# Kernel tuning notes

Measured on AMD Instinct MI355X. Metric: run time of the kernel, lower is better.

## Reference

```python
import jax, jax.numpy as jnp
import numpy as np

N = 20000
E = 320000
HID = 64
HEADS = 4
OUT = 64
NEG_SLOPE = 0.2


def gat_conv(x, src, dst, W, a_src, a_dst, b, heads, out_ch, n_nodes):
    # Linear transform then split heads: [N, heads, out_ch]
    h = (x @ W).reshape(n_nodes, heads, out_ch)
    # Per-node attention logits (PyG GATConv): alpha_i = <h_i, a>
    alpha_s = (h * a_src).sum(-1)  # [N, heads]
    alpha_d = (h * a_dst).sum(-1)  # [N, heads]
    # Edge-wise raw scores e_{j->i} = LeakyReLU(alpha_s[j] + alpha_d[i])
    e = jax.nn.leaky_relu(alpha_s[src] + alpha_d[dst], NEG_SLOPE)  # [E, heads]
    # Segment softmax over incoming edges of each destination node
    m = jax.ops.segment_max(e, dst, num_segments=n_nodes)  # [N, heads]
    ex = jnp.exp(e - m[dst])
    s = jax.ops.segment_sum(ex, dst, num_segments=n_nodes)  # [N, heads]
    alpha = ex / (s[dst] + 1e-16)  # [E, heads]
    # Weighted scatter-add aggregation
    msg = h[src] * alpha[..., None]  # [E, heads, out_ch]
    out = jax.ops.segment_sum(msg, dst, num_segments=n_nodes)
    return out.reshape(n_nodes, heads * out_ch) + b


def setup_inputs() -> dict:
    key = jax.random.key(0)
    ks = jax.random.split(key, 16)
    sc = lambda fi, fo: 1.0 / np.sqrt(fi)
    x = jax.random.normal(ks[0], (N, HID), dtype=jnp.float32)
    edge_index = jax.random.randint(ks[1], (2, E), 0, N, dtype=jnp.int32)
    d = dict(x=x, edge_index=edge_index)
    # layer 1: HID -> HID, HEADS heads (concat)
    d['W1'] = jax.random.normal(ks[2], (HID, HEADS * HID), jnp.float32) * sc(HID, HEADS * HID)
    d['a1s'] = jax.random.normal(ks[3], (HEADS, HID), jnp.float32) * 0.1
    d['a1d'] = jax.random.normal(ks[4], (HEADS, HID), jnp.float32) * 0.1
    d['b1'] = jnp.zeros((HEADS * HID,), jnp.float32)
    # layer 2: HEADS*HID -> HID, HEADS heads (concat)
    d['W2'] = jax.random.normal(ks[5], (HEADS * HID, HEADS * HID), jnp.float32) * sc(HEADS * HID, HEADS * HID)
    d['a2s'] = jax.random.normal(ks[6], (HEADS, HID), jnp.float32) * 0.1
    d['a2d'] = jax.random.normal(ks[7], (HEADS, HID), jnp.float32) * 0.1
    d['b2'] = jnp.zeros((HEADS * HID,), jnp.float32)
    # layer 3: HEADS*HID -> OUT, 1 head
    d['W3'] = jax.random.normal(ks[8], (HEADS * HID, OUT), jnp.float32) * sc(HEADS * HID, OUT)
    d['a3s'] = jax.random.normal(ks[9], (1, OUT), jnp.float32) * 0.1
    d['a3d'] = jax.random.normal(ks[10], (1, OUT), jnp.float32) * 0.1
    d['b3'] = jnp.zeros((OUT,), jnp.float32)
    return d


def reference(x, edge_index, W1, a1s, a1d, b1, W2, a2s, a2d, b2, W3, a3s, a3d, b3):
    src, dst = edge_index[0], edge_index[1]
    h = jax.nn.relu(gat_conv(x, src, dst, W1, a1s, a1d, b1, HEADS, HID, N))
    h = jax.nn.relu(gat_conv(h, src, dst, W2, a2s, a2d, b2, HEADS, HID, N))
    out = gat_conv(h, src, dst, W3, a3s, a3d, b3, 1, OUT, N)
    return out
```

## Files before the change

kernel.cpp:

```cpp
#include <hip/hip_runtime.h>
#include <hip/hip_bf16.h>
#include <hip/hip_fp16.h>
#include <cstdint>

#define HID 64
#define NHEADS 4
#define NEG_SLOPE 0.2f

typedef __attribute__((ext_vector_type(8))) short short8;
typedef __attribute__((ext_vector_type(4))) short short4v;
typedef __attribute__((ext_vector_type(16))) float f32x16;
typedef unsigned short us;

__device__ __forceinline__ us f2bf(float f) {
    unsigned int u = __float_as_uint(f);
    unsigned int r = (u + 0x7FFFu + ((u >> 16) & 1u)) >> 16;
    return (us)r;
}
__device__ __forceinline__ float bf2f(us h) {
    return __uint_as_float(((unsigned int)h) << 16);
}
__device__ __forceinline__ float leaky(float e) {
    return (e > 0.f) ? e : NEG_SLOPE * e;
}

__global__ void histo_kernel(const int* __restrict__ dst, int* __restrict__ counts, int E) {
    int i = blockIdx.x * blockDim.x + threadIdx.x;
    if (i < E) atomicAdd(&counts[dst[i]], 1);
}

__global__ __launch_bounds__(256) void scanA_kernel(const int* __restrict__ counts,
                                                    int* __restrict__ bsum, int n) {
    const int i = blockIdx.x * 256 + threadIdx.x;
    int v = (i < n) ? counts[i] : 0;
#pragma unroll
    for (int o = 32; o; o >>= 1) v += __shfl_xor(v, o);
    __shared__ int ws[4];
    if ((threadIdx.x & 63) == 0) ws[threadIdx.x >> 6] = v;
    __syncthreads();
    if (threadIdx.x == 0) bsum[blockIdx.x] = ws[0] + ws[1] + ws[2] + ws[3];
}

__global__ __launch_bounds__(256) void scanC_kernel(const int* __restrict__ counts,
                                                    const int* __restrict__ bsum,
                                                    int* __restrict__ offs,
                                                    int* __restrict__ wp, int n, int nb) {
    __shared__ int sh[256];
    __shared__ int shb[256];
    const int t = threadIdx.x;
    shb[t] = (t < nb) ? bsum[t] : 0;
    __syncthreads();
    for (int o = 1; o < 256; o <<= 1) {
        int u = (t >= o) ? shb[t - o] : 0;
        __syncthreads();
        shb[t] += u;
        __syncthreads();
    }
    const int base = (blockIdx.x == 0) ? 0 : shb[blockIdx.x - 1];
    const int i = blockIdx.x * 256 + t;
    const int v = (i < n) ? counts[i] : 0;
    sh[t] = v;
    __syncthreads();
    for (int o = 1; o < 256; o <<= 1) {
        int u = (t >= o) ? sh[t - o] : 0;
        __syncthreads();
        sh[t] += u;
        __syncthreads();
    }
    if (i < n) {
        const int off = base + sh[t] - v;
        offs[i] = off;
        wp[i] = off;
        if (i == n - 1) offs[n] = base + sh[t];
    }
}

__global__ void scatter_kernel(const int* __restrict__ src, const int* __restrict__ dst,
                               int* __restrict__ wp, int* __restrict__ csr, int E) {
    int i = blockIdx.x * blockDim.x + threadIdx.x;
    if (i < E) {
        int d = dst[i];
        int p = atomicAdd(&wp[d], 1);
        csr[p] = src[i];
    }
}

__device__ __forceinline__ void wsplit_one(const float* __restrict__ W, us* __restrict__ WTh,
                                           us* __restrict__ WTl, int K, int OUTC, int i) {
    const int c = i / K;
    const int k = i - c * K;
    const float v = W[(size_t)k * OUTC + c];
    const us h = f2bf(v);
    WTh[i] = h;
    WTl[i] = f2bf(v - bf2f(h));
}

__device__ __forceinline__ void vaprep_one(const float* __restrict__ W,
                                           const float* __restrict__ as,
                                           const float* __restrict__ ad,
                                           us* __restrict__ vh, us* __restrict__ vl,
                                           int K, int OUTC, int H, int i) {
    const int j = i / K;
    const int k = i - j * K;
    const int hh = (j < 4) ? j : j - 4;
    const float* a = (j < 4) ? as : ad;
    float acc = 0.f;
    if (hh < H) {
        for (int c = 0; c < 64; ++c)
            acc += W[(size_t)k * OUTC + hh * 64 + c] * a[hh * 64 + c];
    }
    const us h = f2bf(acc);
    vh[i] = h;
    vl[i] = f2bf(acc - bf2f(h));
}

__global__ __launch_bounds__(256) void prep_kernel(
    const float* x, int nx,
    const float* W1, const float* W2, const float* W3,
    const float* a1s, const float* a1d, const float* a2s, const float* a2d,
    const float* a3s, const float* a3d,
    us* xh, us* xl,
    us* wt1h, us* wt1l, us* wt2h, us* wt2l, us* wt3h, us* wt3l,
    us* va1h, us* va1l, us* va2h, us* va2l, us* va3h, us* va3l) {
    int idx = blockIdx.x * 256 + threadIdx.x;
    if (idx < nx) {
        const float v = x[idx];
        const us h = f2bf(v);
        xh[idx] = h;
        xl[idx] = f2bf(v - bf2f(h));
        return;
    }
    idx -= nx;
    if (idx < 16384) { wsplit_one(W1, wt1h, wt1l, 64, 256, idx); return; }
    idx -= 16384;
    if (idx < 65536) { wsplit_one(W2, wt2h, wt2l, 256, 256, idx); return; }
    idx -= 65536;
    if (idx < 16384) { wsplit_one(W3, wt3h, wt3l, 256, 64, idx); return; }
    idx -= 16384;
    if (idx < 512) { vaprep_one(W1, a1s, a1d, va1h, va1l, 64, 256, 4, idx); return; }
    idx -= 512;
    if (idx < 2048) { vaprep_one(W2, a2s, a2d, va2h, va2l, 256, 256, 4, idx); return; }
    idx -= 2048;
    if (idx < 2048) { vaprep_one(W3, a3s, a3d, va3h, va3l, 256, 64, 1, idx); return; }
}

template <int K, int OUTC, int BN, int HA>
__global__ __launch_bounds__(256) void gemm_mfma_kernel(const us* __restrict__ AH,
                                                        const us* __restrict__ AL,
                                                        const us* __restrict__ WTh,
                                                        const us* __restrict__ WTl,
                                                        const us* __restrict__ vah,
                                                        const us* __restrict__ val,
                                                        _Float16* __restrict__ H16,
                                                        float* __restrict__ alpha_s,
                                                        float* __restrict__ alpha_d, int nrows) {
    constexpr int CGS = BN / 64;
    constexpr int NB = BN / 64;
    constexpr int TPC = 4 / NB;
    __shared__ short Ah[2 * 64 * 32];
    __shared__ short Al[2 * 64 * 32];
    __shared__ short Bh[2 * BN * 32];
    __shared__ short Bl[2 * BN * 32];
    __shared__ short Vh[2 * 8 * 32];
    __shared__ short Vl[2 * 8 * 32];

    const int tid = threadIdx.x;
    const int lane = tid & 63;
    const int wid = tid >> 6;
    const int wr = wid >> 1;
    const int wc = wid & 1;
    const int r31 = lane & 31;
    const int khw = lane >> 5;
    const int row0 = blockIdx.x * 64;
    const int c0 = blockIdx.y * BN;
    const bool alpha_blk = (blockIdx.y == 0);
    const bool alpha_wave = alpha_blk && (wc == 0);

    const int ar = tid >> 2;
    const int akb = tid & 3;
    const bool aok = (row0 + ar) < nrows;
    const int bcol = tid / TPC;
    const int bkb = (tid % TPC) * NB;

    f32x16 acc[CGS];
#pragma unroll
    for (int cg = 0; cg < CGS; ++cg)
#pragma unroll
        for (int r = 0; r < 16; ++r) acc[cg][r] = 0.f;
    f32x16 accv;
#pragma unroll
    for (int r = 0; r < 16; ++r) accv[r] = 0.f;

    for (int k0 = 0; k0 < K; k0 += 64) {
        __syncthreads();
#pragma unroll
        for (int sub = 0; sub < 2; ++sub) {
            {
                short8 h = {}, l = {};
                if (aok) {
                    const size_t so = (size_t)(row0 + ar) * K + k0 + sub * 32 + akb * 8;
                    h = *reinterpret_cast<const short8*>(&AH[so]);
                    l = *reinterpret_cast<const short8*>(&AL[so]);
                }
                const int off = sub * 2048 + ar * 32 + ((akb ^ (ar & 3)) << 3);
                *reinterpret_cast<short8*>(&Ah[off]) = h;
                *reinterpret_cast<short8*>(&Al[off]) = l;
            }
            {
                const us* srcH = &WTh[(size_t)(c0 + bcol) * K + k0 + sub * 32];
                const us* srcL = &WTl[(size_t)(c0 + bcol) * K + k0 + sub * 32];
#pragma unroll
                for (int b = 0; b < NB; ++b) {
                    short8 h = *reinterpret_cast<const short8*>(&srcH[(bkb + b) * 8]);
                    short8 l = *reinterpret_cast<const short8*>(&srcL[(bkb + b) * 8]);
                    const int off = sub * BN * 32 + bcol * 32 + (((bkb + b) ^ (bcol & 3)) << 3);
                    *reinterpret_cast<short8*>(&Bh[off]) = h;
                    *reinterpret_cast<short8*>(&Bl[off]) = l;
                }
            }
            if (alpha_blk && tid < 32) {
                const int col = tid >> 2, kb2 = tid & 3;
                const int off = sub * 256 + col * 32 + kb2 * 8;
                *reinterpret_cast<short8*>(&Vh[off]) =
                    *reinterpret_cast<const short8*>(&vah[col * K + k0 + sub * 32 + kb2 * 8]);
                *reinterpret_cast<short8*>(&Vl[off]) =
                    *reinterpret_cast<const short8*>(&val[col * K + k0 + sub * 32 + kb2 * 8]);
            }
        }
        __syncthreads();
#pragma unroll
        for (int sub = 0; sub < 2; ++sub) {
#pragma unroll
            for (int ks = 0; ks < 32; ks += 16) {
                const int kb = (ks >> 3) + khw;
                const int aoff = sub * 2048 + (wr * 32 + r31) * 32 + ((kb ^ (r31 & 3)) << 3);
                short8 ah = *reinterpret_cast<const short8*>(&Ah[aoff]);
                short8 al = *reinterpret_cast<const short8*>(&Al[aoff]);
#pragma unroll
                for (int cg = 0; cg < CGS; ++cg) {
                    const int coll = wc * (BN / 2) + cg * 32 + r31;
                    const int boff = sub * BN * 32 + coll * 32 + ((kb ^ (r31 & 3)) << 3);
                    short8 bh = *reinterpret_cast<const short8*>(&Bh[boff]);
                    short8 bl = *reinterpret_cast<const short8*>(&Bl[boff]);
                    acc[cg] = __builtin_amdgcn_mfma_f32_32x32x16_bf16(ah, bh, acc[cg], 0, 0, 0);
                    acc[cg] = __builtin_amdgcn_mfma_f32_32x32x16_bf16(ah, bl, acc[cg], 0, 0, 0);
                    acc[cg] = __builtin_amdgcn_mfma_f32_32x32x16_bf16(al, bh, acc[cg], 0, 0, 0);
                }
                if (alpha_wave) {
                    short8 vh = {}, vl = {};
                    if (r31 < 8) {
                        const int voff = sub * 256 + r31 * 32 + (kb << 3);
                        vh = *reinterpret_cast<const short8*>(&Vh[voff]);
                        vl = *reinterpret_cast<const short8*>(&Vl[voff]);
                    }
                    accv = __builtin_amdgcn_mfma_f32_32x32x16_bf16(ah, vh, accv, 0, 0, 0);
                    accv = __builtin_amdgcn_mfma_f32_32x32x16_bf16(ah, vl, accv, 0, 0, 0);
                    accv = __builtin_amdgcn_mfma_f32_32x32x16_bf16(al, vh, accv, 0, 0, 0);
                }
            }
        }
    }

#pragma unroll
    for (int cg = 0; cg < CGS; ++cg) {
#pragma unroll
        for (int reg = 0; reg < 16; ++reg) {
            const int row = row0 + wr * 32 + (reg & 3) + 8 * (reg >> 2) + 4 * khw;
            if (row < nrows) {
                const int col = c0 + wc * (BN / 2) + cg * 32 + r31;
                H16[(size_t)row * OUTC + col] = (_Float16)acc[cg][reg];
            }
        }
    }
    if (alpha_wave && r31 < 8) {
        const int hsel = r31 & 3;
        if (hsel < HA) {
            float* dstp = (r31 < 4) ? alpha_s : alpha_d;
#pragma unroll
            for (int reg = 0; reg < 16; ++reg) {
                const int row = row0 + wr * 32 + (reg & 3) + 8 * (reg >> 2) + 4 * khw;
                if (row < nrows) dstp[(size_t)row * HA + hsel] = accv[reg];
            }
        }
    }
}

__global__ __launch_bounds__(64) void maxagg4_kernel(const _Float16* __restrict__ h,
                                                     const float* __restrict__ alpha_s,
                                                     const float* __restrict__ alpha_d,
                                                     const int* __restrict__ offs,
                                                     const int* __restrict__ csr,
                                                     float* __restrict__ w,
                                                     const float* __restrict__ bias,
                                                     us* __restrict__ outH,
                                                     us* __restrict__ outL, int n_nodes) {
    __shared__ float wsh[64 * 4];
    const int gw = blockIdx.x;
    const int lane = threadIdx.x;
    if (gw >= n_nodes) return;
    const int start = offs[gw];
    const int end = offs[gw + 1];
    const int deg = end - start;
    const float4 ad = *reinterpret_cast<const float4*>(&alpha_d[(size_t)gw * 4]);
    const int head = lane >> 4;
    const int cb = lane << 2;
    float4 r;
    float4 acc = make_float4(0.f, 0.f, 0.f, 0.f);

    if (deg <= 64) {
        const int i = start + lane;
        const bool has = i < end;
        int s_reg = 0;
        float4 e = make_float4(0.f, 0.f, 0.f, 0.f);
        float4 m = make_float4(-INFINITY, -INFINITY, -INFINITY, -INFINITY);
        if (has) {
            s_reg = csr[i];
            const float4 a = *reinterpret_cast<const float4*>(&alpha_s[(size_t)s_reg * 4]);
            e.x = leaky(a.x + ad.x);
            e.y = leaky(a.y + ad.y);
            e.z = leaky(a.z + ad.z);
            e.w = leaky(a.w + ad.w);
            m = e;
        }
#pragma unroll
        for (int o = 32; o; o >>= 1) {
            m.x = fmaxf(m.x, __shfl_xor(m.x, o));
            m.y = fmaxf(m.y, __shfl_xor(m.y, o));
            m.z = fmaxf(m.z, __shfl_xor(m.z, o));
            m.w = fmaxf(m.w, __shfl_xor(m.w, o));
        }
        float4 ex = make_float4(0.f, 0.f, 0.f, 0.f);
        if (has) {
            ex.x = __expf(e.x - m.x);
            ex.y = __expf(e.y - m.y);
            ex.z = __expf(e.z - m.z);
            ex.w = __expf(e.w - m.w);
        }
        float4 sum = ex;
#pragma unroll
        for (int o = 32; o; o >>= 1) {
            sum.x += __shfl_xor(sum.x, o);
            sum.y += __shfl_xor(sum.y, o);
            sum.z += __shfl_xor(sum.z, o);
            sum.w += __shfl_xor(sum.w, o);
        }
        r.x = 1.f / (sum.x + 1e-16f);
        r.y = 1.f / (sum.y + 1e-16f);
        r.z = 1.f / (sum.z + 1e-16f);
        r.w = 1.f / (sum.w + 1e-16f);
        *reinterpret_cast<float4*>(&wsh[lane * 4]) = ex;
        const int degr = (deg + 7) & ~7;
        for (int j = 0; j < degr; j += 8) {
#pragma unroll
            for (int u = 0; u < 8; ++u) {
                const int s = __shfl(s_reg, j + u);
                const float wv = wsh[(j + u) * 4 + head];
                const uint2 uv = *reinterpret_cast<const uint2*>(&h[(size_t)s * 256 + cb]);
                const float2 f0 = __half22float2(__builtin_bit_cast(__half2, uv.x));
                const float2 f1 = __half22float2(__builtin_bit_cast(__half2, uv.y));
                acc.x = fmaf(wv, f0.x, acc.x);
                acc.y = fmaf(wv, f0.y, acc.y);
                acc.z = fmaf(wv, f1.x, acc.z);
                acc.w = fmaf(wv, f1.y, acc.w);
            }
        }
    } else {
        float4 m = make_float4(-INFINITY, -INFINITY, -INFINITY, -INFINITY);
        float4 sum = make_float4(0.f, 0.f, 0.f, 0.f);
        for (int i = start + lane; i < end; i += 64) {
            const int s = csr[i];
            const float4 a = *reinterpret_cast<const float4*>(&alpha_s[(size_t)s * 4]);
            float4 e;
            e.x = leaky(a.x + ad.x);
            e.y = leaky(a.y + ad.y);
            e.z = leaky(a.z + ad.z);
            e.w = leaky(a.w + ad.w);
            *reinterpret_cast<float4*>(&w[(size_t)i * 4]) = e;
            m.x = fmaxf(m.x, e.x);
            m.y = fmaxf(m.y, e.y);
            m.z = fmaxf(m.z, e.z);
            m.w = fmaxf(m.w, e.w);
        }
#pragma unroll
        for (int o = 32; o; o >>= 1) {
            m.x = fmaxf(m.x, __shfl_xor(m.x, o));
            m.y = fmaxf(m.y, __shfl_xor(m.y, o));
            m.z = fmaxf(m.z, __shfl_xor(m.z, o));
            m.w = fmaxf(m.w, __shfl_xor(m.w, o));
        }
        for (int i = start + lane; i < end; i += 64) {
            float4 e = *reinterpret_cast<float4*>(&w[(size_t)i * 4]);
            e.x = __expf(e.x - m.x);
            e.y = __expf(e.y - m.y);
            e.z = __expf(e.z - m.z);
            e.w = __expf(e.w - m.w);
            *reinterpret_cast<float4*>(&w[(size_t)i * 4]) = e;
            sum.x += e.x;
            sum.y += e.y;
            sum.z += e.z;
            sum.w += e.w;
        }
#pragma unroll
        for (int o = 32; o; o >>= 1) {
            sum.x += __shfl_xor(sum.x, o);
            sum.y += __shfl_xor(sum.y, o);
            sum.z += __shfl_xor(sum.z, o);
            sum.w += __shfl_xor(sum.w, o);
        }
        r.x = 1.f / (sum.x + 1e-16f);
        r.y = 1.f / (sum.y + 1e-16f);
        r.z = 1.f / (sum.z + 1e-16f);
        r.w = 1.f / (sum.w + 1e-16f);
        for (int i = start; i < end; ++i) {
            const int s = csr[i];
            const float4 w0 = *reinterpret_cast<const float4*>(&w[(size_t)i * 4]);
            const float wv = head == 0 ? w0.x : head == 1 ? w0.y : head == 2 ? w0.z : w0.w;
            const uint2 uv = *reinterpret_cast<const uint2*>(&h[(size_t)s * 256 + cb]);
            const float2 f0 = __half22float2(__builtin_bit_cast(__half2, uv.x));
            const float2 f1 = __half22float2(__builtin_bit_cast(__half2, uv.y));
            acc.x = fmaf(wv, f0.x, acc.x);
            acc.y = fmaf(wv, f0.y, acc.y);
            acc.z = fmaf(wv, f1.x, acc.z);
            acc.w = fmaf(wv, f1.y, acc.w);
        }
    }

    const float rv = head == 0 ? r.x : head == 1 ? r.y : head == 2 ? r.z : r.w;
    const float4 b4 = *reinterpret_cast<const float4*>(&bias[cb]);
    float o0 = fmaxf(acc.x * rv + b4.x, 0.f);
    float o1 = fmaxf(acc.y * rv + b4.y, 0.f);
    float o2 = fmaxf(acc.z * rv + b4.z, 0.f);
    float o3 = fmaxf(acc.w * rv + b4.w, 0.f);
    short4v oh, ol;
    us t;
    t = f2bf(o0); oh[0] = (short)t; ol[0] = (short)f2bf(o0 - bf2f(t));
    t = f2bf(o1); oh[1] = (short)t; ol[1] = (short)f2bf(o1 - bf2f(t));
    t = f2bf(o2); oh[2] = (short)t; ol[2] = (short)f2bf(o2 - bf2f(t));
    t = f2bf(o3); oh[3] = (short)t; ol[3] = (short)f2bf(o3 - bf2f(t));
    *reinterpret_cast<short4v*>(&outH[(size_t)gw * 256 + cb]) = oh;
    *reinterpret_cast<short4v*>(&outL[(size_t)gw * 256 + cb]) = ol;
}

__global__ __launch_bounds__(64) void maxagg1_kernel(const _Float16* __restrict__ h,
                                                     const float* __restrict__ alpha_s,
                                                     const float* __restrict__ alpha_d,
                                                     const int* __restrict__ offs,
                                                     const int* __restrict__ csr,
                                                     float* __restrict__ w,
                                                     const float* __restrict__ bias,
                                                     float* __restrict__ out, int n_nodes) {
    const int gw = blockIdx.x;
    const int lane = threadIdx.x;
    if (gw >= n_nodes) return;
    const int start = offs[gw];
    const int end = offs[gw + 1];
    const int deg = end - start;
    const float ad = alpha_d[gw];
    float r;
    float acc = 0.f;

    if (deg <= 64) {
        const int i = start + lane;
        const bool has = i < end;
        int s_reg = 0;
        float e = 0.f, m = -INFINITY;
        if (has) {
            s_reg = csr[i];
            e = leaky(alpha_s[s_reg] + ad);
            m = e;
        }
#pragma unroll
        for (int o = 32; o; o >>= 1) m = fmaxf(m, __shfl_xor(m, o));
        float ex = has ? __expf(e - m) : 0.f;
        float sum = ex;
#pragma unroll
        for (int o = 32; o; o >>= 1) sum += __shfl_xor(sum, o);
        r = 1.f / (sum + 1e-16f);
        const int degr = (deg + 7) & ~7;
        for (int j = 0; j < degr; j += 8) {
#pragma unroll
            for (int u = 0; u < 8; ++u) {
                const int s = __shfl(s_reg, j + u);
                const float wv = __shfl(ex, j + u);
                acc = fmaf(wv, (float)h[(size_t)s * 64 + lane], acc);
            }
        }
    } else {
        float m = -INFINITY, sum = 0.f;
        for (int i = start + lane; i < end; i += 64) {
            const float e = leaky(alpha_s[csr[i]] + ad);
            w[i] = e;
            m = fmaxf(m, e);
        }
#pragma unroll
        for (int o = 32; o; o >>= 1) m = fmaxf(m, __shfl_xor(m, o));
        for (int i = start + lane; i < end; i += 64) {
            const float ex = __expf(w[i] - m);
            w[i] = ex;
            sum += ex;
        }
#pragma unroll
        for (int o = 32; o; o >>= 1) sum += __shfl_xor(sum, o);
        r = 1.f / (sum + 1e-16f);
        for (int i = start; i < end; ++i)
            acc = fmaf(w[i], (float)h[(size_t)csr[i] * 64 + lane], acc);
    }
    float o = acc * r + bias[lane];
    out[(size_t)gw * 64 + lane] = o;
}

extern "C" void kernel_launch(void* const* d_in, const int* in_sizes, int n_in,
                              void* d_out, int out_size, void* d_ws, size_t ws_size,
                              hipStream_t stream) {
    const float* x   = (const float*)d_in[0];
    const int*   ei  = (const int*)d_in[1];
    const float* W1  = (const float*)d_in[2];
    const float* a1s = (const float*)d_in[3];
    const float* a1d = (const float*)d_in[4];
    const float* b1  = (const float*)d_in[5];
    const float* W2  = (const float*)d_in[6];
    const float* a2s = (const float*)d_in[7];
    const float* a2d = (const float*)d_in[8];
    const float* b2  = (const float*)d_in[9];
    const float* W3  = (const float*)d_in[10];
    const float* a3s = (const float*)d_in[11];
    const float* a3d = (const float*)d_in[12];
    const float* b3  = (const float*)d_in[13];
    float* out = (float*)d_out;

    const int N = in_sizes[0] / HID;
    const int E = in_sizes[1] / 2;
    const int* src = ei;
    const int* dst = ei + E;

    char* p = (char*)d_ws;
    auto alloc = [&](size_t bytes) {
        char* q = p;
        p += (bytes + 255) & ~(size_t)255;
        return q;
    };
    _Float16* h16 = (_Float16*)alloc((size_t)N * 256 * 2);
    us* xh  = (us*)alloc((size_t)N * 64 * 2);
    us* xl  = (us*)alloc((size_t)N * 64 * 2);
    us* g1h = (us*)alloc((size_t)N * 256 * 2);
    us* g1l = (us*)alloc((size_t)N * 256 * 2);
    us* g2h = (us*)alloc((size_t)N * 256 * 2);
    us* g2l = (us*)alloc((size_t)N * 256 * 2);
    float* alpS = (float*)alloc((size_t)N * NHEADS * 4);
    float* alpD = (float*)alloc((size_t)N * NHEADS * 4);
    float* wbuf = (float*)alloc((size_t)E * NHEADS * 4);
    int* counts = (int*)alloc((size_t)N * 4);
    int* offs   = (int*)alloc((size_t)(N + 1) * 4);
    int* wp     = (int*)alloc((size_t)N * 4);
    int* csr    = (int*)alloc((size_t)E * 4);
    int* bsum   = (int*)alloc((size_t)256 * 4);
    us* wt1h = (us*)alloc((size_t)64 * 256 * 2);
    us* wt1l = (us*)alloc((size_t)64 * 256 * 2);
    us* wt2h = (us*)alloc((size_t)256 * 256 * 2);
    us* wt2l = (us*)alloc((size_t)256 * 256 * 2);
    us* wt3h = (us*)alloc((size_t)256 * 64 * 2);
    us* wt3l = (us*)alloc((size_t)256 * 64 * 2);
    us* va1h = (us*)alloc((size_t)8 * 64 * 2);
    us* va1l = (us*)alloc((size_t)8 * 64 * 2);
    us* va2h = (us*)alloc((size_t)8 * 256 * 2);
    us* va2l = (us*)alloc((size_t)8 * 256 * 2);
    us* va3h = (us*)alloc((size_t)8 * 256 * 2);
    us* va3l = (us*)alloc((size_t)8 * 256 * 2);

    hipMemsetAsync(counts, 0, (size_t)N * 4, stream);
    const int eb = (E + 255) / 256;
    const int nb = (N + 255) / 256;
    histo_kernel<<<eb, 256, 0, stream>>>(dst, counts, E);
    scanA_kernel<<<nb, 256, 0, stream>>>(counts, bsum, N);
    scanC_kernel<<<nb, 256, 0, stream>>>(counts, bsum, offs, wp, N, nb);
    scatter_kernel<<<eb, 256, 0, stream>>>(src, dst, wp, csr, E);

    const int nx = N * 64;
    const int ptotal = nx + 102912;
    prep_kernel<<<(ptotal + 255) / 256, 256, 0, stream>>>(
        x, nx, W1, W2, W3, a1s, a1d, a2s, a2d, a3s, a3d,
        xh, xl, wt1h, wt1l, wt2h, wt2l, wt3h, wt3l,
        va1h, va1l, va2h, va2l, va3h, va3l);

    const int gb64 = (N + 63) / 64;

    gemm_mfma_kernel<64, 256, 128, 4><<<dim3(gb64, 2), 256, 0, stream>>>(
        xh, xl, wt1h, wt1l, va1h, va1l, h16, alpS, alpD, N);
    maxagg4_kernel<<<N, 64, 0, stream>>>(h16, alpS, alpD, offs, csr, wbuf, b1, g1h, g1l, N);

    gemm_mfma_kernel<256, 256, 128, 4><<<dim3(gb64, 2), 256, 0, stream>>>(
        g1h, g1l, wt2h, wt2l, va2h, va2l, h16, alpS, alpD, N);
    maxagg4_kernel<<<N, 64, 0, stream>>>(h16, alpS, alpD, offs, csr, wbuf, b2, g2h, g2l, N);

    gemm_mfma_kernel<256, 64, 64, 1><<<dim3(gb64, 1), 256, 0, stream>>>(
        g2h, g2l, wt3h, wt3l, va3h, va3l, h16, alpS, alpD, N);
    maxagg1_kernel<<<N, 64, 0, stream>>>(h16, alpS, alpD, offs, csr, wbuf, b3, out, N);
}
```

Measured before the change: 166.4 us.

## Split 4-head aggregation across two wavefronts per node with XCD-aware block mapping

The multi-head aggregation kernel now launches two 64-lane blocks per destination node, each handling two of the four heads (128 channels), so every lane processes 2 channels instead of 4. Block indices are remapped so the two halves of a node's work land on different XCD groups (blocks b and b+4 within each group of 8), while consecutive nodes in each half share an XCD for L2 locality of the gathered rows. This doubles parallelism and shortens per-block dependency chains, at the cost of computing the softmax setup (CSR reads, alpha gathers, shuffles) twice per node and issuing narrower 4-byte gathers.

```diff
diff --git a/kernel.cpp b/kernel.cpp
--- a/kernel.cpp
+++ b/kernel.cpp
@@ -294,151 +294,122 @@
                                                      const float* __restrict__ bias,
                                                      us* __restrict__ outH,
                                                      us* __restrict__ outL, int n_nodes) {
-    __shared__ float wsh[64 * 4];
-    const int gw = blockIdx.x;
+    __shared__ float wsh[64 * 2];
+    const int b = blockIdx.x;
+    const int xcd = b & 7;
+    const int half = xcd >> 2;
+    const int gw = ((b >> 3) << 2) + (xcd & 3);
     const int lane = threadIdx.x;
     if (gw >= n_nodes) return;
     const int start = offs[gw];
     const int end = offs[gw + 1];
     const int deg = end - start;
-    const float4 ad = *reinterpret_cast<const float4*>(&alpha_d[(size_t)gw * 4]);
-    const int head = lane >> 4;
-    const int cb = lane << 2;
-    float4 r;
-    float4 acc = make_float4(0.f, 0.f, 0.f, 0.f);
+    const float2 ad = *reinterpret_cast<const float2*>(&alpha_d[(size_t)gw * 4 + half * 2]);
+    const int sub = lane >> 5;
+    const size_t hbase = (size_t)half * 128 + lane * 2;
+    float2 r;
+    float2 acc = make_float2(0.f, 0.f);
 
     if (deg <= 64) {
         const int i = start + lane;
         const bool has = i < end;
         int s_reg = 0;
-        float4 e = make_float4(0.f, 0.f, 0.f, 0.f);
-        float4 m = make_float4(-INFINITY, -INFINITY, -INFINITY, -INFINITY);
+        float2 e = make_float2(0.f, 0.f);
+        float2 m = make_float2(-INFINITY, -INFINITY);
         if (has) {
             s_reg = csr[i];
-            const float4 a = *reinterpret_cast<const float4*>(&alpha_s[(size_t)s_reg * 4]);
+            const float2 a = *reinterpret_cast<const float2*>(&alpha_s[(size_t)s_reg * 4 + half * 2]);
             e.x = leaky(a.x + ad.x);
             e.y = leaky(a.y + ad.y);
-            e.z = leaky(a.z + ad.z);
-            e.w = leaky(a.w + ad.w);
             m = e;
         }
 #pragma unroll
         for (int o = 32; o; o >>= 1) {
             m.x = fmaxf(m.x, __shfl_xor(m.x, o));
             m.y = fmaxf(m.y, __shfl_xor(m.y, o));
-            m.z = fmaxf(m.z, __shfl_xor(m.z, o));
-            m.w = fmaxf(m.w, __shfl_xor(m.w, o));
-        }
-        float4 ex = make_float4(0.f, 0.f, 0.f, 0.f);
+        }
+        float2 ex = make_float2(0.f, 0.f);
         if (has) {
             ex.x = __expf(e.x - m.x);
             ex.y = __expf(e.y - m.y);
-            ex.z = __expf(e.z - m.z);
-            ex.w = __expf(e.w - m.w);
-        }
-        float4 sum = ex;
+        }
+        float2 sum = ex;
 #pragma unroll
         for (int o = 32; o; o >>= 1) {
             sum.x += __shfl_xor(sum.x, o);
             sum.y += __shfl_xor(sum.y, o);
-            sum.z += __shfl_xor(sum.z, o);
-            sum.w += __shfl_xor(sum.w, o);
         }
         r.x = 1.f / (sum.x + 1e-16f);
         r.y = 1.f / (sum.y + 1e-16f);
-        r.z = 1.f / (sum.z + 1e-16f);
-        r.w = 1.f / (sum.w + 1e-16f);
-        *reinterpret_cast<float4*>(&wsh[lane * 4]) = ex;
+        *reinterpret_cast<float2*>(&wsh[lane * 2]) = ex;
         const int degr = (deg + 7) & ~7;
         for (int j = 0; j < degr; j += 8) {
 #pragma unroll
             for (int u = 0; u < 8; ++u) {
                 const int s = __shfl(s_reg, j + u);
-                const float wv = wsh[(j + u) * 4 + head];
-                const uint2 uv = *reinterpret_cast<const uint2*>(&h[(size_t)s * 256 + cb]);
-                const float2 f0 = __half22float2(__builtin_bit_cast(__half2, uv.x));
-                const float2 f1 = __half22float2(__builtin_bit_cast(__half2, uv.y));
-                acc.x = fmaf(wv, f0.x, acc.x);
-                acc.y = fmaf(wv, f0.y, acc.y);
-                acc.z = fmaf(wv, f1.x, acc.z);
-                acc.w = fmaf(wv, f1.y, acc.w);
+                const float wv = wsh[(j + u) * 2 + sub];
+                const unsigned int uv =
+                    *reinterpret_cast<const unsigned int*>(&h[(size_t)s * 256 + hbase]);
+                const float2 f = __half22float2(__builtin_bit_cast(__half2, uv));
+                acc.x = fmaf(wv, f.x, acc.x);
+                acc.y = fmaf(wv, f.y, acc.y);
             }
         }
     } else {
-        float4 m = make_float4(-INFINITY, -INFINITY, -INFINITY, -INFINITY);
-        float4 sum = make_float4(0.f, 0.f, 0.f, 0.f);
+        float2 m = make_float2(-INFINITY, -INFINITY);
+        float2 sum = make_float2(0.f, 0.f);
         for (int i = start + lane; i < end; i += 64) {
             const int s = csr[i];
-            const float4 a = *reinterpret_cast<const float4*>(&alpha_s[(size_t)s * 4]);
-            float4 e;
+            const float2 a = *reinterpret_cast<const float2*>(&alpha_s[(size_t)s * 4 + half * 2]);
+            float2 e;
             e.x = leaky(a.x + ad.x);
             e.y = leaky(a.y + ad.y);
-            e.z = leaky(a.z + ad.z);
-            e.w = leaky(a.w + ad.w);
-            *reinterpret_cast<float4*>(&w[(size_t)i * 4]) = e;
+            *reinterpret_cast<float2*>(&w[(size_t)i * 4 + half * 2]) = e;
             m.x = fmaxf(m.x, e.x);
             m.y = fmaxf(m.y, e.y);
-            m.z = fmaxf(m.z, e.z);
-            m.w = fmaxf(m.w, e.w);
         }
 #pragma unroll
         for (int o = 32; o; o >>= 1) {
             m.x = fmaxf(m.x, __shfl_xor(m.x, o));
             m.y = fmaxf(m.y, __shfl_xor(m.y, o));
-            m.z = fmaxf(m.z, __shfl_xor(m.z, o));
-            m.w = fmaxf(m.w, __shfl_xor(m.w, o));
         }
         for (int i = start + lane; i < end; i += 64) {
-            float4 e = *reinterpret_cast<float4*>(&w[(size_t)i * 4]);
+            float2 e = *reinterpret_cast<float2*>(&w[(size_t)i * 4 + half * 2]);
             e.x = __expf(e.x - m.x);
             e.y = __expf(e.y - m.y);
-            e.z = __expf(e.z - m.z);
-            e.w = __expf(e.w - m.w);
-            *reinterpret_cast<float4*>(&w[(size_t)i * 4]) = e;
+            *reinterpret_cast<float2*>(&w[(size_t)i * 4 + half * 2]) = e;
             sum.x += e.x;
             sum.y += e.y;
-            sum.z += e.z;
-            sum.w += e.w;
         }
 #pragma unroll
         for (int o = 32; o; o >>= 1) {
             sum.x += __shfl_xor(sum.x, o);
             sum.y += __shfl_xor(sum.y, o);
-            sum.z += __shfl_xor(sum.z, o);
-            sum.w += __shfl_xor(sum.w, o);
         }
         r.x = 1.f / (sum.x + 1e-16f);
         r.y = 1.f / (sum.y + 1e-16f);
-        r.z = 1.f / (sum.z + 1e-16f);
-        r.w = 1.f / (sum.w + 1e-16f);
         for (int i = start; i < end; ++i) {
             const int s = csr[i];
-            const float4 w0 = *reinterpret_cast<const float4*>(&w[(size_t)i * 4]);
-            const float wv = head == 0 ? w0.x : head == 1 ? w0.y : head == 2 ? w0.z : w0.w;
-            const uint2 uv = *reinterpret_cast<const uint2*>(&h[(size_t)s * 256 + cb]);
-            const float2 f0 = __half22float2(__builtin_bit_cast(__half2, uv.x));
-            const float2 f1 = __half22float2(__builtin_bit_cast(__half2, uv.y));
-            acc.x = fmaf(wv, f0.x, acc.x);
-            acc.y = fmaf(wv, f0.y, acc.y);
-            acc.z = fmaf(wv, f1.x, acc.z);
-            acc.w = fmaf(wv, f1.y, acc.w);
-        }
-    }
-
-    const float rv = head == 0 ? r.x : head == 1 ? r.y : head == 2 ? r.z : r.w;
-    const float4 b4 = *reinterpret_cast<const float4*>(&bias[cb]);
-    float o0 = fmaxf(acc.x * rv + b4.x, 0.f);
-    float o1 = fmaxf(acc.y * rv + b4.y, 0.f);
-    float o2 = fmaxf(acc.z * rv + b4.z, 0.f);
-    float o3 = fmaxf(acc.w * rv + b4.w, 0.f);
-    short4v oh, ol;
-    us t;
-    t = f2bf(o0); oh[0] = (short)t; ol[0] = (short)f2bf(o0 - bf2f(t));
-    t = f2bf(o1); oh[1] = (short)t; ol[1] = (short)f2bf(o1 - bf2f(t));
-    t = f2bf(o2); oh[2] = (short)t; ol[2] = (short)f2bf(o2 - bf2f(t));
-    t = f2bf(o3); oh[3] = (short)t; ol[3] = (short)f2bf(o3 - bf2f(t));
-    *reinterpret_cast<short4v*>(&outH[(size_t)gw * 256 + cb]) = oh;
-    *reinterpret_cast<short4v*>(&outL[(size_t)gw * 256 + cb]) = ol;
+            const float2 wv2 = *reinterpret_cast<const float2*>(&w[(size_t)i * 4 + half * 2]);
+            const float wv = sub == 0 ? wv2.x : wv2.y;
+            const unsigned int uv =
+                *reinterpret_cast<const unsigned int*>(&h[(size_t)s * 256 + hbase]);
+            const float2 f = __half22float2(__builtin_bit_cast(__half2, uv));
+            acc.x = fmaf(wv, f.x, acc.x);
+            acc.y = fmaf(wv, f.y, acc.y);
+        }
+    }
+
+    const float rv = sub == 0 ? r.x : r.y;
+    const float2 b2 = *reinterpret_cast<const float2*>(&bias[hbase]);
+    float o0 = fmaxf(acc.x * rv + b2.x, 0.f);
+    float o1 = fmaxf(acc.y * rv + b2.y, 0.f);
+    us h0 = f2bf(o0), h1 = f2bf(o1);
+    us l0 = f2bf(o0 - bf2f(h0)), l1 = f2bf(o1 - bf2f(h1));
+    const unsigned int packH = (unsigned int)h0 | ((unsigned int)h1 << 16);
+    const unsigned int packL = (unsigned int)l0 | ((unsigned int)l1 << 16);
+    *reinterpret_cast<unsigned int*>(&outH[(size_t)gw * 256 + hbase]) = packH;
+    *reinterpret_cast<unsigned int*>(&outL[(size_t)gw * 256 + hbase]) = packL;
 }
 
 __global__ __launch_bounds__(64) void maxagg1_kernel(const _Float16* __restrict__ h,
@@ -583,14 +554,15 @@
         va1h, va1l, va2h, va2l, va3h, va3l);
 
     const int gb64 = (N + 63) / 64;
+    const int aggb = ((N + 3) / 4) * 8;
 
     gemm_mfma_kernel<64, 256, 128, 4><<<dim3(gb64, 2), 256, 0, stream>>>(
         xh, xl, wt1h, wt1l, va1h, va1l, h16, alpS, alpD, N);
-    maxagg4_kernel<<<N, 64, 0, stream>>>(h16, alpS, alpD, offs, csr, wbuf, b1, g1h, g1l, N);
+    maxagg4_kernel<<<aggb, 64, 0, stream>>>(h16, alpS, alpD, offs, csr, wbuf, b1, g1h, g1l, N);
 
     gemm_mfma_kernel<256, 256, 128, 4><<<dim3(gb64, 2), 256, 0, stream>>>(
         g1h, g1l, wt2h, wt2l, va2h, va2l, h16, alpS, alpD, N);
-    maxagg4_kernel<<<N, 64, 0, stream>>>(h16, alpS, alpD, offs, csr, wbuf, b2, g2h, g2l, N);
+    maxagg4_kernel<<<aggb, 64, 0, stream>>>(h16, alpS, alpD, offs, csr, wbuf, b2, g2h, g2l, N);
 
     gemm_mfma_kernel<256, 64, 64, 1><<<dim3(gb64, 1), 256, 0, stream>>>(
         g2h, g2l, wt3h, wt3l, va3h, va3l, h16, alpS, alpD, N);
```

Result: slower. 172.1 us (+3.4%).
